# Optimization experiments

Measured on AMD Instinct MI355X. Metric: run time of the kernel, lower is better.

The kernel has to match this reference:

```python
import jax, jax.numpy as jnp
import numpy as np

HEADS = 16  # init_kwargs['heads']


def setup_inputs() -> dict:
    key = jax.random.key(0)
    k1, k2, k3, k4, k5, k6 = jax.random.split(key, 6)
    N, L, E = 2, 2048, 1024
    return {
        "values": jax.random.normal(k1, (N, L, E), dtype=jnp.float32),
        "key": jax.random.normal(k2, (N, L, E), dtype=jnp.float32),
        "query": jax.random.normal(k3, (N, L, E), dtype=jnp.float32),
        "mask": jax.random.randint(k4, (N, 1, L, L), 0, 2, dtype=jnp.int32),
        # fc_out: Linear(heads*head_dim=E, E) with bias
        "W_out": jax.random.normal(k5, (E, E), dtype=jnp.float32) / np.sqrt(E),
        "b_out": jax.random.normal(k6, (E,), dtype=jnp.float32) * 0.01,
    }


def reference(values, key, query, mask, W_out, b_out):
    N, Lq, E = query.shape
    Lk = key.shape[1]
    H = HEADS
    D = E // H  # head_dim = 64
    q = query.reshape(N, Lq, H, D)
    k = key.reshape(N, Lk, H, D)
    v = values.reshape(N, Lk, H, D)
    # energy: (N, H, Q, K)
    energy = jnp.einsum("nqhd,nkhd->nhqk", q, k)
    # masked_fill BEFORE scaling, as in the original
    energy = jnp.where(mask == 0, jnp.float32(-1e20), energy)
    attn = jax.nn.softmax(energy / np.float32(np.sqrt(D)), axis=3)
    out = jnp.einsum("nhqk,nkhd->nqhd", attn, v).reshape(N, Lq, H * D)
    return out @ W_out.T + b_out
```

## Files before the change

### kernel.cpp

```cpp
#include <hip/hip_runtime.h>

#define L_SEQ  2048
#define EMB    1024
#define NHEAD  16
#define HDIM   64
#define NBATCH 2

typedef unsigned short u16;
typedef unsigned long long u64;
typedef short bf16x8 __attribute__((ext_vector_type(8)));
typedef float f32x4  __attribute__((ext_vector_type(4)));

static __device__ __forceinline__ u16 f2bf(float x) {
    union { float f; unsigned u; } a; a.f = x;
    unsigned r = a.u + 0x7FFFu + ((a.u >> 16) & 1u);
    return (u16)(r >> 16);
}
static __device__ __forceinline__ void cvt8(const float4& a, const float4& b, u16* o, float s) {
    o[0]=f2bf(a.x*s); o[1]=f2bf(a.y*s); o[2]=f2bf(a.z*s); o[3]=f2bf(a.w*s);
    o[4]=f2bf(b.x*s); o[5]=f2bf(b.y*s); o[6]=f2bf(b.z*s); o[7]=f2bf(b.w*s);
}

__global__ void pack_mask(const int* __restrict__ Mg, u64* __restrict__ maskp)
{
    const int wave = threadIdx.x >> 6;
    const int lane = threadIdx.x & 63;
    const int row  = blockIdx.x * 4 + wave;
    const int* mp = Mg + (size_t)row * L_SEQ + lane;
    u64* op = maskp + (size_t)row * (L_SEQ / 64);
    for (int t = 0; t < L_SEQ / 64; ++t) {
        u64 b = __ballot(mp[t * 64] != 0);
        if (lane == 0) op[t] = b;
    }
}

__global__ __launch_bounds__(256)
void prep_qkv(const float* __restrict__ Qg, const float* __restrict__ Kg,
              const float* __restrict__ Vg, u16* __restrict__ Qb,
              u16* __restrict__ Kb, u16* __restrict__ Vt)
{
    const int t = blockIdx.x, h = blockIdx.y, n = blockIdx.z;
    const int tid = threadIdx.x;
    const int row = tid >> 2;
    const int dc  = (tid & 3) * 16;

    __shared__ u16 Vl2[64][72];

    const size_t gin = ((size_t)(n * L_SEQ) + t * 64 + row) * EMB + h * HDIM + dc;

    {
        u16 o[16];
        cvt8(*(const float4*)(Qg + gin),     *(const float4*)(Qg + gin + 4),  o,     0.125f);
        cvt8(*(const float4*)(Qg + gin + 8), *(const float4*)(Qg + gin + 12), o + 8, 0.125f);
        *(uint4*)(Qb + gin)     = *(const uint4*)o;
        *(uint4*)(Qb + gin + 8) = *(const uint4*)&o[8];
    }
    {
        u16 o[16];
        cvt8(*(const float4*)(Kg + gin),     *(const float4*)(Kg + gin + 4),  o,     1.f);
        cvt8(*(const float4*)(Kg + gin + 8), *(const float4*)(Kg + gin + 12), o + 8, 1.f);
        size_t ko = ((size_t)(n * NHEAD + h) * L_SEQ + t * 64 + row) * HDIM + dc;
        *(uint4*)(Kb + ko)     = *(const uint4*)o;
        *(uint4*)(Kb + ko + 8) = *(const uint4*)&o[8];
    }
    {
        u16 o[16];
        cvt8(*(const float4*)(Vg + gin),     *(const float4*)(Vg + gin + 4),  o,     1.f);
        cvt8(*(const float4*)(Vg + gin + 8), *(const float4*)(Vg + gin + 12), o + 8, 1.f);
        #pragma unroll
        for (int j = 0; j < 16; ++j) Vl2[dc + j][row] = o[j];
    }
    __syncthreads();
    {
        const int d  = tid >> 2;
        const int kc = (tid & 3) * 16;
        size_t vo = ((size_t)(n * NHEAD + h) * HDIM + d) * L_SEQ + t * 64 + kc;
        *(uint4*)(Vt + vo)     = *(const uint4*)&Vl2[d][kc];
        *(uint4*)(Vt + vo + 8) = *(const uint4*)&Vl2[d][kc + 8];
    }
}

__global__ void wcvt(const float* __restrict__ W, u16* __restrict__ Wb)
{
    int i = (blockIdx.x * 256 + threadIdx.x) * 8;
    float4 a = *(const float4*)(W + i);
    float4 b = *(const float4*)(W + i + 4);
    u16 o[8];
    cvt8(a, b, o, 1.f);
    *(uint4*)(Wb + i) = *(const uint4*)o;
}

__global__ __launch_bounds__(256, 4)
void attn_kernel(const u16* __restrict__ Qb, const u16* __restrict__ Kb,
                 const u16* __restrict__ Vt, const u64* __restrict__ maskp,
                 u16* __restrict__ Og)
{
    const int qblk = blockIdx.x;
    const int h    = blockIdx.y;
    const int n    = blockIdx.z;
    const int tid  = threadIdx.x;
    const int wave = tid >> 6;
    const int lane = tid & 63;
    const int l16  = lane & 15;
    const int quad = lane >> 4;

    __shared__ u16 Kl[64][72];
    __shared__ u16 Vl[64][72];
    __shared__ u16 Pl[4][16][72];

    const int q0 = qblk * 64 + wave * 16;

    bf16x8 qf[2];
    {
        const u16* qp = Qb + ((size_t)(n * L_SEQ) + q0 + l16) * EMB + h * HDIM;
        qf[0] = *(const bf16x8*)(qp + quad * 8);
        qf[1] = *(const bf16x8*)(qp + 32 + quad * 8);
    }

    f32x4 acc[4];
    #pragma unroll
    for (int c = 0; c < 4; ++c)
        #pragma unroll
        for (int r = 0; r < 4; ++r) acc[c][r] = 0.f;
    float lsum[4] = {0.f, 0.f, 0.f, 0.f};

    const u16* kbase = Kb + (size_t)(n * NHEAD + h) * L_SEQ * HDIM;
    const u16* vbase = Vt + (size_t)(n * NHEAD + h) * HDIM * L_SEQ;
    const u64* mbase = maskp + ((size_t)(n * L_SEQ) + q0 + quad * 4) * (L_SEQ / 64);

    const int srow = tid >> 2;
    const int scol = (tid & 3) * 16;

    uint4 kr0, kr1, vr0, vr1;
    u64 mr[4];

    {
        const u16* kp = kbase + (size_t)srow * HDIM + scol;
        const u16* vp = vbase + (size_t)srow * L_SEQ + scol;
        kr0 = *(const uint4*)kp;  kr1 = *(const uint4*)(kp + 8);
        vr0 = *(const uint4*)vp;  vr1 = *(const uint4*)(vp + 8);
        #pragma unroll
        for (int r = 0; r < 4; ++r) mr[r] = mbase[(size_t)r * (L_SEQ / 64)];
    }

    for (int t = 0; t < L_SEQ / 64; ++t) {
        __syncthreads();
        *(uint4*)&Kl[srow][scol]     = kr0;
        *(uint4*)&Kl[srow][scol + 8] = kr1;
        *(uint4*)&Vl[srow][scol]     = vr0;
        *(uint4*)&Vl[srow][scol + 8] = vr1;
        u64 mcur[4];
        #pragma unroll
        for (int r = 0; r < 4; ++r) mcur[r] = mr[r];

        if (t + 1 < L_SEQ / 64) {
            const u16* kp = kbase + (size_t)((t + 1) * 64 + srow) * HDIM + scol;
            const u16* vp = vbase + (size_t)srow * L_SEQ + (t + 1) * 64 + scol;
            kr0 = *(const uint4*)kp;  kr1 = *(const uint4*)(kp + 8);
            vr0 = *(const uint4*)vp;  vr1 = *(const uint4*)(vp + 8);
            #pragma unroll
            for (int r = 0; r < 4; ++r) mr[r] = mbase[(size_t)r * (L_SEQ / 64) + t + 1];
        }
        __syncthreads();

        f32x4 S[4];
        #pragma unroll
        for (int cc = 0; cc < 4; ++cc) {
            bf16x8 b0 = *(const bf16x8*)&Kl[cc * 16 + l16][quad * 8];
            bf16x8 b1 = *(const bf16x8*)&Kl[cc * 16 + l16][32 + quad * 8];
            f32x4 z; z[0]=0.f; z[1]=0.f; z[2]=0.f; z[3]=0.f;
            z = __builtin_amdgcn_mfma_f32_16x16x32_bf16(qf[0], b0, z, 0, 0, 0);
            z = __builtin_amdgcn_mfma_f32_16x16x32_bf16(qf[1], b1, z, 0, 0, 0);
            S[cc] = z;
        }

        #pragma unroll
        for (int cc = 0; cc < 4; ++cc) {
            #pragma unroll
            for (int r = 0; r < 4; ++r) {
                float s = ((mcur[r] >> (cc * 16 + l16)) & 1ull) ? S[cc][r] : -1.0e20f;
                float p = __expf(s - 16.f);
                S[cc][r] = p;
                lsum[r] += p;
            }
        }

        #pragma unroll
        for (int cc = 0; cc < 4; ++cc)
            #pragma unroll
            for (int r = 0; r < 4; ++r)
                Pl[wave][quad * 4 + r][cc * 16 + l16] = f2bf(S[cc][r]);

        asm volatile("s_waitcnt lgkmcnt(0)" ::: "memory");

        #pragma unroll
        for (int kc = 0; kc < 2; ++kc) {
            bf16x8 pf = *(const bf16x8*)&Pl[wave][l16][kc * 32 + quad * 8];
            #pragma unroll
            for (int dc = 0; dc < 4; ++dc) {
                bf16x8 vf = *(const bf16x8*)&Vl[dc * 16 + l16][kc * 32 + quad * 8];
                acc[dc] = __builtin_amdgcn_mfma_f32_16x16x32_bf16(pf, vf, acc[dc], 0, 0, 0);
            }
        }
    }

    #pragma unroll
    for (int r = 0; r < 4; ++r) {
        float s = lsum[r];
        s += __shfl_xor(s, 1);
        s += __shfl_xor(s, 2);
        s += __shfl_xor(s, 4);
        s += __shfl_xor(s, 8);
        float inv = 1.f / s;
        u16* op = Og + ((size_t)(n * L_SEQ) + q0 + quad * 4 + r) * EMB + h * HDIM;
        #pragma unroll
        for (int dc = 0; dc < 4; ++dc)
            op[dc * 16 + l16] = f2bf(acc[dc][r] * inv);
    }
}

__global__ __launch_bounds__(256, 4)
void out_gemm(const u16* __restrict__ A, const u16* __restrict__ B,
              const float* __restrict__ bias, float* __restrict__ out)
{
    const int bn  = blockIdx.x;
    const int bm  = blockIdx.y;
    const int tid = threadIdx.x;
    const int wave = tid >> 6;
    const int lane = tid & 63;
    const int l16  = lane & 15;
    const int quad = lane >> 4;
    const int wr = wave >> 1, wc = wave & 1;

    __shared__ u16 Al[64][72];
    __shared__ u16 Bl[64][72];

    f32x4 acc[2][2];
    #pragma unroll
    for (int i = 0; i < 2; ++i)
        #pragma unroll
        for (int j = 0; j < 2; ++j)
            #pragma unroll
            for (int r = 0; r < 4; ++r) acc[i][j][r] = 0.f;

    const int srow = tid >> 2;
    const int kc   = (tid & 3) * 16;

    const u16* ap = A + (size_t)(bm * 64 + srow) * EMB + kc;
    const u16* bp = B + (size_t)(bn * 64 + srow) * EMB + kc;

    uint4 ar0 = *(const uint4*)ap,        ar1 = *(const uint4*)(ap + 8);
    uint4 br0 = *(const uint4*)bp,        br1 = *(const uint4*)(bp + 8);

    for (int k0 = 0; k0 < EMB; k0 += 64) {
        __syncthreads();
        *(uint4*)&Al[srow][kc]     = ar0;
        *(uint4*)&Al[srow][kc + 8] = ar1;
        *(uint4*)&Bl[srow][kc]     = br0;
        *(uint4*)&Bl[srow][kc + 8] = br1;
        if (k0 + 64 < EMB) {
            ar0 = *(const uint4*)(ap + k0 + 64);  ar1 = *(const uint4*)(ap + k0 + 72);
            br0 = *(const uint4*)(bp + k0 + 64);  br1 = *(const uint4*)(bp + k0 + 72);
        }
        __syncthreads();

        #pragma unroll
        for (int kk = 0; kk < 2; ++kk) {
            bf16x8 af[2], bfr[2];
            #pragma unroll
            for (int i = 0; i < 2; ++i)
                af[i] = *(const bf16x8*)&Al[wr * 32 + i * 16 + l16][kk * 32 + quad * 8];
            #pragma unroll
            for (int j = 0; j < 2; ++j)
                bfr[j] = *(const bf16x8*)&Bl[wc * 32 + j * 16 + l16][kk * 32 + quad * 8];
            #pragma unroll
            for (int i = 0; i < 2; ++i)
                #pragma unroll
                for (int j = 0; j < 2; ++j)
                    acc[i][j] = __builtin_amdgcn_mfma_f32_16x16x32_bf16(af[i], bfr[j], acc[i][j], 0, 0, 0);
        }
    }

    #pragma unroll
    for (int j = 0; j < 2; ++j) {
        int col = bn * 64 + wc * 32 + j * 16 + l16;
        float bv = bias[col];
        #pragma unroll
        for (int i = 0; i < 2; ++i) {
            int row0 = bm * 64 + wr * 32 + i * 16 + quad * 4;
            #pragma unroll
            for (int r = 0; r < 4; ++r)
                out[(size_t)(row0 + r) * EMB + col] = acc[i][j][r] + bv;
        }
    }
}

extern "C" void kernel_launch(void* const* d_in, const int* in_sizes, int n_in,
                              void* d_out, int out_size, void* d_ws, size_t ws_size,
                              hipStream_t stream)
{
    const float* Vg = (const float*)d_in[0];
    const float* Kg = (const float*)d_in[1];
    const float* Qg = (const float*)d_in[2];
    const int*   Mg = (const int*)d_in[3];
    const float* Wg = (const float*)d_in[4];
    const float* Bg = (const float*)d_in[5];
    float* Og = (float*)d_out;

    const size_t QKV = (size_t)NBATCH * L_SEQ * EMB;
    char* ws = (char*)d_ws;
    u16* attn_ws = (u16*)ws;
    u16* Wb      = (u16*)(ws + QKV * 2);
    u16* Qb      = (u16*)(ws + QKV * 2 + 2 * 1024 * 1024);
    u16* Kb      = Qb + QKV;
    u16* Vt      = Kb + QKV;
    u64* maskp   = (u64*)(Vt + QKV);

    pack_mask<<<dim3(NBATCH * L_SEQ / 4), 256, 0, stream>>>(Mg, maskp);
    prep_qkv<<<dim3(L_SEQ / 64, NHEAD, NBATCH), 256, 0, stream>>>(Qg, Kg, Vg, Qb, Kb, Vt);
    wcvt<<<dim3(EMB * EMB / (256 * 8)), 256, 0, stream>>>(Wg, Wb);

    dim3 g1(L_SEQ / 64, NHEAD, NBATCH);
    attn_kernel<<<g1, 256, 0, stream>>>(Qb, Kb, Vt, maskp, attn_ws);

    dim3 g2(EMB / 64, (NBATCH * L_SEQ) / 64);
    out_gemm<<<g2, 256, 0, stream>>>(attn_ws, Wb, Bg, Og);
}
```

Before: 236.2 us.

## Transpose QK MFMA so P stays in registers via permlane swaps

Swaps the MFMA operand order so the score tile comes out transposed, with each lane holding one query row. The probabilities are then packed to bf16 with v_cvt_pk_bf16_f32 and rearranged into the PV operand layout with permlane32/16 swaps, which removes the shared-memory round trip for P. The log2(e) factor is folded into the Q prescale so the kernel can call exp2 directly, and masking becomes a bitwise AND. This cuts LDS traffic, the per-element mask shifts and the reduction shuffles, and it allows packed output stores. It relies on gfx950-specific instructions and on the fixed offset of 16 being dropped, which risks overflow on large scores.

```diff
diff --git a/kernel.cpp b/kernel.cpp
--- a/kernel.cpp
+++ b/kernel.cpp
@@ -7,9 +7,11 @@
 #define NBATCH 2
 
 typedef unsigned short u16;
+typedef unsigned int   u32;
 typedef unsigned long long u64;
 typedef short bf16x8 __attribute__((ext_vector_type(8)));
 typedef float f32x4  __attribute__((ext_vector_type(4)));
+typedef int   i32x4  __attribute__((ext_vector_type(4)));
 
 static __device__ __forceinline__ u16 f2bf(float x) {
     union { float f; unsigned u; } a; a.f = x;
@@ -19,6 +21,18 @@
 static __device__ __forceinline__ void cvt8(const float4& a, const float4& b, u16* o, float s) {
     o[0]=f2bf(a.x*s); o[1]=f2bf(a.y*s); o[2]=f2bf(a.z*s); o[3]=f2bf(a.w*s);
     o[4]=f2bf(b.x*s); o[5]=f2bf(b.y*s); o[6]=f2bf(b.z*s); o[7]=f2bf(b.w*s);
+}
+
+static __device__ __forceinline__ u32 cvt_pk_bf16(float lo, float hi) {
+    u32 r;
+    asm("v_cvt_pk_bf16_f32 %0, %1, %2" : "=v"(r) : "v"(lo), "v"(hi));
+    return r;
+}
+static __device__ __forceinline__ void permswap32(u32 &x, u32 &y) {
+    asm("v_permlane32_swap_b32 %0, %1" : "+v"(x), "+v"(y));
+}
+static __device__ __forceinline__ void permswap16(u32 &x, u32 &y) {
+    asm("v_permlane16_swap_b32 %0, %1" : "+v"(x), "+v"(y));
 }
 
 __global__ void pack_mask(const int* __restrict__ Mg, u64* __restrict__ maskp)
@@ -49,9 +63,10 @@
     const size_t gin = ((size_t)(n * L_SEQ) + t * 64 + row) * EMB + h * HDIM + dc;
 
     {
+        const float qs = 0.125f * 1.44269504f;
         u16 o[16];
-        cvt8(*(const float4*)(Qg + gin),     *(const float4*)(Qg + gin + 4),  o,     0.125f);
-        cvt8(*(const float4*)(Qg + gin + 8), *(const float4*)(Qg + gin + 12), o + 8, 0.125f);
+        cvt8(*(const float4*)(Qg + gin),     *(const float4*)(Qg + gin + 4),  o,     qs);
+        cvt8(*(const float4*)(Qg + gin + 8), *(const float4*)(Qg + gin + 12), o + 8, qs);
         *(uint4*)(Qb + gin)     = *(const uint4*)o;
         *(uint4*)(Qb + gin + 8) = *(const uint4*)&o[8];
     }
@@ -106,7 +121,6 @@
 
     __shared__ u16 Kl[64][72];
     __shared__ u16 Vl[64][72];
-    __shared__ u16 Pl[4][16][72];
 
     const int q0 = qblk * 64 + wave * 16;
 
@@ -122,25 +136,24 @@
     for (int c = 0; c < 4; ++c)
         #pragma unroll
         for (int r = 0; r < 4; ++r) acc[c][r] = 0.f;
-    float lsum[4] = {0.f, 0.f, 0.f, 0.f};
+    float lsum = 0.f;
 
     const u16* kbase = Kb + (size_t)(n * NHEAD + h) * L_SEQ * HDIM;
     const u16* vbase = Vt + (size_t)(n * NHEAD + h) * HDIM * L_SEQ;
-    const u64* mbase = maskp + ((size_t)(n * L_SEQ) + q0 + quad * 4) * (L_SEQ / 64);
+    const u64* mbase = maskp + ((size_t)(n * L_SEQ) + q0 + l16) * (L_SEQ / 64);
 
     const int srow = tid >> 2;
     const int scol = (tid & 3) * 16;
 
     uint4 kr0, kr1, vr0, vr1;
-    u64 mr[4];
+    u64 mr;
 
     {
         const u16* kp = kbase + (size_t)srow * HDIM + scol;
         const u16* vp = vbase + (size_t)srow * L_SEQ + scol;
         kr0 = *(const uint4*)kp;  kr1 = *(const uint4*)(kp + 8);
         vr0 = *(const uint4*)vp;  vr1 = *(const uint4*)(vp + 8);
-        #pragma unroll
-        for (int r = 0; r < 4; ++r) mr[r] = mbase[(size_t)r * (L_SEQ / 64)];
+        mr  = mbase[0];
     }
 
     for (int t = 0; t < L_SEQ / 64; ++t) {
@@ -149,73 +162,77 @@
         *(uint4*)&Kl[srow][scol + 8] = kr1;
         *(uint4*)&Vl[srow][scol]     = vr0;
         *(uint4*)&Vl[srow][scol + 8] = vr1;
-        u64 mcur[4];
-        #pragma unroll
-        for (int r = 0; r < 4; ++r) mcur[r] = mr[r];
+        u64 mcur = mr;
 
         if (t + 1 < L_SEQ / 64) {
             const u16* kp = kbase + (size_t)((t + 1) * 64 + srow) * HDIM + scol;
             const u16* vp = vbase + (size_t)srow * L_SEQ + (t + 1) * 64 + scol;
             kr0 = *(const uint4*)kp;  kr1 = *(const uint4*)(kp + 8);
             vr0 = *(const uint4*)vp;  vr1 = *(const uint4*)(vp + 8);
-            #pragma unroll
-            for (int r = 0; r < 4; ++r) mr[r] = mbase[(size_t)r * (L_SEQ / 64) + t + 1];
+            mr  = mbase[t + 1];
         }
         __syncthreads();
 
-        f32x4 S[4];
+        f32x4 St[4];
         #pragma unroll
         for (int cc = 0; cc < 4; ++cc) {
-            bf16x8 b0 = *(const bf16x8*)&Kl[cc * 16 + l16][quad * 8];
-            bf16x8 b1 = *(const bf16x8*)&Kl[cc * 16 + l16][32 + quad * 8];
+            bf16x8 k0 = *(const bf16x8*)&Kl[cc * 16 + l16][quad * 8];
+            bf16x8 k1 = *(const bf16x8*)&Kl[cc * 16 + l16][32 + quad * 8];
             f32x4 z; z[0]=0.f; z[1]=0.f; z[2]=0.f; z[3]=0.f;
-            z = __builtin_amdgcn_mfma_f32_16x16x32_bf16(qf[0], b0, z, 0, 0, 0);
-            z = __builtin_amdgcn_mfma_f32_16x16x32_bf16(qf[1], b1, z, 0, 0, 0);
-            S[cc] = z;
-        }
-
+            z = __builtin_amdgcn_mfma_f32_16x16x32_bf16(k0, qf[0], z, 0, 0, 0);
+            z = __builtin_amdgcn_mfma_f32_16x16x32_bf16(k1, qf[1], z, 0, 0, 0);
+            St[cc] = z;
+        }
+
+        u32 lo  = (u32)(mcur >> (quad * 4));
+        u32 hiw = (u32)(mcur >> (quad * 4 + 32));
+        u32 Dw[8];
         #pragma unroll
         for (int cc = 0; cc < 4; ++cc) {
+            u32 w = (cc < 2) ? lo : hiw;
+            float pv[4];
             #pragma unroll
             for (int r = 0; r < 4; ++r) {
-                float s = ((mcur[r] >> (cc * 16 + l16)) & 1ull) ? S[cc][r] : -1.0e20f;
-                float p = __expf(s - 16.f);
-                S[cc][r] = p;
-                lsum[r] += p;
+                const int pos = (cc & 1) * 16 + r;
+                int sm = (int)(w << (31 - pos)) >> 31;
+                float p = __builtin_amdgcn_exp2f(St[cc][r]);
+                p = __int_as_float(__float_as_int(p) & sm);
+                lsum += p;
+                pv[r] = p;
             }
-        }
-
-        #pragma unroll
-        for (int cc = 0; cc < 4; ++cc)
-            #pragma unroll
-            for (int r = 0; r < 4; ++r)
-                Pl[wave][quad * 4 + r][cc * 16 + l16] = f2bf(S[cc][r]);
-
-        asm volatile("s_waitcnt lgkmcnt(0)" ::: "memory");
+            Dw[2 * cc]     = cvt_pk_bf16(pv[0], pv[1]);
+            Dw[2 * cc + 1] = cvt_pk_bf16(pv[2], pv[3]);
+        }
 
         #pragma unroll
         for (int kc = 0; kc < 2; ++kc) {
-            bf16x8 pf = *(const bf16x8*)&Pl[wave][l16][kc * 32 + quad * 8];
+            u32 b0 = Dw[4 * kc + 0], b2 = Dw[4 * kc + 2];
+            permswap32(b0, b2); permswap16(b0, b2);
+            u32 b1 = Dw[4 * kc + 1], b3 = Dw[4 * kc + 3];
+            permswap32(b1, b3); permswap16(b1, b3);
+            union { i32x4 i; bf16x8 v; } pu;
+            pu.i[0] = (int)b0; pu.i[1] = (int)b1; pu.i[2] = (int)b2; pu.i[3] = (int)b3;
+            bf16x8 pf = pu.v;
             #pragma unroll
             for (int dc = 0; dc < 4; ++dc) {
                 bf16x8 vf = *(const bf16x8*)&Vl[dc * 16 + l16][kc * 32 + quad * 8];
-                acc[dc] = __builtin_amdgcn_mfma_f32_16x16x32_bf16(pf, vf, acc[dc], 0, 0, 0);
+                acc[dc] = __builtin_amdgcn_mfma_f32_16x16x32_bf16(vf, pf, acc[dc], 0, 0, 0);
             }
         }
     }
 
+    float s = lsum;
+    s += __shfl_xor(s, 16);
+    s += __shfl_xor(s, 32);
+    float inv = 1.f / s;
+
+    u16* op = Og + ((size_t)(n * L_SEQ) + q0 + l16) * EMB + h * HDIM + quad * 4;
     #pragma unroll
-    for (int r = 0; r < 4; ++r) {
-        float s = lsum[r];
-        s += __shfl_xor(s, 1);
-        s += __shfl_xor(s, 2);
-        s += __shfl_xor(s, 4);
-        s += __shfl_xor(s, 8);
-        float inv = 1.f / s;
-        u16* op = Og + ((size_t)(n * L_SEQ) + q0 + quad * 4 + r) * EMB + h * HDIM;
-        #pragma unroll
-        for (int dc = 0; dc < 4; ++dc)
-            op[dc * 16 + l16] = f2bf(acc[dc][r] * inv);
+    for (int dc = 0; dc < 4; ++dc) {
+        u32 u0 = cvt_pk_bf16(acc[dc][0] * inv, acc[dc][1] * inv);
+        u32 u1 = cvt_pk_bf16(acc[dc][2] * inv, acc[dc][3] * inv);
+        uint2 st; st.x = u0; st.y = u1;
+        *(uint2*)(op + dc * 16) = st;
     }
 }
 
```

Result: faster. 220.5 us (-6.6%).
